# Kernel tuning notes

Hardware: AMD Instinct MI355X
Metric: run time of the kernel (lower is better)

Reference implementation:

```python
import jax, jax.numpy as jnp
import numpy as np

T_REFRAC = 2  # t_refrac init kwarg


def setup_inputs() -> dict:
    key = jax.random.key(0)
    B, T, N = 16, 256, 8192
    x = jax.random.uniform(key, (B, T, N), dtype=jnp.float32)
    return {"x": x}


def reference(x) -> jnp.ndarray:
    """SpikingCell with track_spikes, enable_clamp, t_refrac=2, buffer_dv,
    reset_mechanism='subtract', accumulate_only=False.
    Concrete hooks: _compute_dv = identity, _count_spikes = sum over features.
    Keras RNN initializes all states to zeros.
    Returns the per-timestep spike outputs [B, T, N]."""
    B, T, N = x.shape
    v0 = jnp.zeros((B, N), x.dtype)        # membrane potential
    sc0 = jnp.zeros((B,), x.dtype)         # spike counter
    clamp0 = jnp.zeros((B,), x.dtype)      # clamp countdown
    refrac0 = jnp.zeros((B, N), x.dtype)   # refractory counters
    buf0 = jnp.zeros((B, N), x.dtype)      # one-step dv buffer

    def step(carry, x_t):
        v, sc, clamp, refrac, dv_buf = carry
        dv = x_t  # _compute_dv = identity
        # buffer_dv: integrate previous step's dv
        dvi = dv_buf
        # _filter_update: clamp gate (layer-global per batch) then refractory gate
        dvi = dvi * (clamp[:, None] <= 0.0).astype(dvi.dtype)
        dvi = dvi * (refrac >= T_REFRAC).astype(dvi.dtype)
        v = v + dvi
        out = (v >= 1.0).astype(v.dtype)
        v = v - out  # reset by subtraction
        sc = sc + jnp.sum(x_t, axis=-1)  # _count_spikes = sum over features
        clamp = clamp - 1.0
        refrac = (refrac + 1.0) * (out == 0.0).astype(refrac.dtype)
        return (v, sc, clamp, refrac, dv), out

    x_tbn = jnp.transpose(x, (1, 0, 2))  # [T, B, N]
    _, outs = jax.lax.scan(step, (v0, sc0, clamp0, refrac0, buf0), x_tbn)
    return jnp.transpose(outs, (1, 0, 2))  # [B, T, N]
```

## Files before the change

### kernel.cpp

```cpp
#include <hip/hip_runtime.h>


constexpr int B = 16;
constexpr int T = 256;
constexpr int N = 8192;

__global__ __launch_bounds__(256) void spiking_kernel(
    const float* __restrict__ x, float* __restrict__ out) {
  const int c = blockIdx.x * blockDim.x + threadIdx.x;
  const int cols = N / 2;
  const int b = c / cols;
  const int n2 = c - b * cols;

  const float2* __restrict__ xp =
      reinterpret_cast<const float2*>(x + (size_t)b * T * N) + n2;
  float2* __restrict__ op =
      reinterpret_cast<float2*>(out + (size_t)b * T * N) + n2;

  float2 v = {0.f, 0.f};
  float2 refrac = {0.f, 0.f};
  float2 buf = {0.f, 0.f};

#pragma unroll 8
  for (int t = 0; t < T; ++t) {
    const float2 xt = xp[(size_t)t * cols];
    float2 o;

    float dvi = (refrac.x >= 2.0f) ? buf.x : 0.0f;
    v.x += dvi;
    o.x = (v.x >= 1.0f) ? 1.0f : 0.0f;
    v.x -= o.x;
    refrac.x = (o.x == 0.0f) ? (refrac.x + 1.0f) : 0.0f;
    buf.x = xt.x;

    dvi = (refrac.y >= 2.0f) ? buf.y : 0.0f;
    v.y += dvi;
    o.y = (v.y >= 1.0f) ? 1.0f : 0.0f;
    v.y -= o.y;
    refrac.y = (o.y == 0.0f) ? (refrac.y + 1.0f) : 0.0f;
    buf.y = xt.y;

    op[(size_t)t * cols] = o;
  }
}

extern "C" void kernel_launch(void* const* d_in, const int* in_sizes, int n_in,
                              void* d_out, int out_size, void* d_ws,
                              size_t ws_size, hipStream_t stream) {
  const float* x = (const float*)d_in[0];
  float* out = (float*)d_out;

  const int threads = 256;
  const int total = B * N / 2;
  const int blocks = total / threads;
  spiking_kernel<<<blocks, threads, 0, stream>>>(x, out);
}
```

Measured before the change: 229.5 us.

## Use one column per thread with register double-buffered prefetch of input timesteps

Each thread now handles a single feature column instead of a float2 pair, which doubles the thread count to 131072. The time loop is split into groups of 16 steps, and the next group's inputs are loaded into registers while the current group is computed. This is meant to hide load latency on what is a memory-bound sequential scan. The cost is more registers per thread, narrower scalar loads and stores, and a launch-bounds occupancy hint.

```diff
diff --git a/kernel.cpp b/kernel.cpp
--- a/kernel.cpp
+++ b/kernel.cpp
@@ -4,43 +4,55 @@
 constexpr int B = 16;
 constexpr int T = 256;
 constexpr int N = 8192;
+constexpr int U = 16;
 
-__global__ __launch_bounds__(256) void spiking_kernel(
+__global__ __launch_bounds__(256, 2) void spiking_kernel(
     const float* __restrict__ x, float* __restrict__ out) {
   const int c = blockIdx.x * blockDim.x + threadIdx.x;
-  const int cols = N / 2;
-  const int b = c / cols;
-  const int n2 = c - b * cols;
+  const int b = c >> 13;
+  const int n = c & (N - 1);
 
-  const float2* __restrict__ xp =
-      reinterpret_cast<const float2*>(x + (size_t)b * T * N) + n2;
-  float2* __restrict__ op =
-      reinterpret_cast<float2*>(out + (size_t)b * T * N) + n2;
+  const float* __restrict__ xp = x + (size_t)b * T * N + n;
+  float* __restrict__ op = out + (size_t)b * T * N + n;
 
-  float2 v = {0.f, 0.f};
-  float2 refrac = {0.f, 0.f};
-  float2 buf = {0.f, 0.f};
+  float v = 0.f, refrac = 0.f, buf = 0.f;
 
-#pragma unroll 8
-  for (int t = 0; t < T; ++t) {
-    const float2 xt = xp[(size_t)t * cols];
-    float2 o;
+  float cur[U], nxt[U];
 
-    float dvi = (refrac.x >= 2.0f) ? buf.x : 0.0f;
-    v.x += dvi;
-    o.x = (v.x >= 1.0f) ? 1.0f : 0.0f;
-    v.x -= o.x;
-    refrac.x = (o.x == 0.0f) ? (refrac.x + 1.0f) : 0.0f;
-    buf.x = xt.x;
+#pragma unroll
+  for (int u = 0; u < U; ++u) cur[u] = xp[(size_t)u * N];
 
-    dvi = (refrac.y >= 2.0f) ? buf.y : 0.0f;
-    v.y += dvi;
-    o.y = (v.y >= 1.0f) ? 1.0f : 0.0f;
-    v.y -= o.y;
-    refrac.y = (o.y == 0.0f) ? (refrac.y + 1.0f) : 0.0f;
-    buf.y = xt.y;
+  for (int g = 0; g < T / U - 1; ++g) {
+    const size_t base_next = (size_t)(g + 1) * U * N;
+#pragma unroll
+    for (int u = 0; u < U; ++u) nxt[u] = xp[base_next + (size_t)u * N];
 
-    op[(size_t)t * cols] = o;
+    const size_t base_cur = (size_t)g * U * N;
+#pragma unroll
+    for (int u = 0; u < U; ++u) {
+      const float dvi = (refrac >= 2.0f) ? buf : 0.0f;
+      v += dvi;
+      const float o = (v >= 1.0f) ? 1.0f : 0.0f;
+      v -= o;
+      refrac = (o == 0.0f) ? (refrac + 1.0f) : 0.0f;
+      buf = cur[u];
+      op[base_cur + (size_t)u * N] = o;
+    }
+
+#pragma unroll
+    for (int u = 0; u < U; ++u) cur[u] = nxt[u];
+  }
+
+  const size_t base_last = (size_t)(T - U) * N;
+#pragma unroll
+  for (int u = 0; u < U; ++u) {
+    const float dvi = (refrac >= 2.0f) ? buf : 0.0f;
+    v += dvi;
+    const float o = (v >= 1.0f) ? 1.0f : 0.0f;
+    v -= o;
+    refrac = (o == 0.0f) ? (refrac + 1.0f) : 0.0f;
+    buf = cur[u];
+    op[base_last + (size_t)u * N] = o;
   }
 }
 
@@ -51,7 +63,7 @@
   float* out = (float*)d_out;
 
   const int threads = 256;
-  const int total = B * N / 2;
+  const int total = B * N;
   const int blocks = total / threads;
   spiking_kernel<<<blocks, threads, 0, stream>>>(x, out);
 }
```

After: 232.3 us. Within noise of the previous version (+1.2%).
